# Kernel optimization log

Hardware: AMD Instinct MI355X
Metric: run time of the kernel (lower is better)

## Reference

```python
import jax, jax.numpy as jnp
import numpy as np

KERNEL_SIZE = 2  # matches init kernel_size
EPS = 1e-6


def setup_inputs() -> dict:
    key = jax.random.key(0)
    x = jax.random.uniform(key, (8, 64, 256, 256), dtype=jnp.float32)
    return {"x": x}


def reference(x) -> jnp.ndarray:
    k = KERNEL_SIZE
    b, c, h, w = x.shape
    hp, wp = h - k + 1, w - k + 1  # stride-1 unfold output dims
    n = k * k
    # Gather the k*k shifted views (equivalent to unfold(2,k,1).unfold(3,k,1)).
    # Fixed small loop over k*k offsets, not over data dims.
    windows = jnp.stack(
        [x[:, :, i:i + hp, j:j + wp] for i in range(k) for j in range(k)],
        axis=-1,
    )  # (b, c, hp, wp, n)
    windows = windows.reshape(b, c, hp * wp, n)
    p = windows / (jnp.sum(windows, axis=-1, keepdims=True) + EPS)
    ent = -jnp.sum(p * jnp.log(p + EPS), axis=-1)  # (b, c, hp*wp)
    return ent
```

## Files before the change

### kernel.cpp

```cpp
#include <hip/hip_runtime.h>

#define H    256
#define W    256
#define HP   255
#define WP   255
#define PIX  (HP * WP)
#define NBC  512
#define EPS  1e-6f
#define LN2  0.69314718055994531f

#define TPI   8192
#define NBLK  (NBC * TPI / 256)
#define BPI   32

typedef float f4 __attribute__((ext_vector_type(4)));

__device__ __forceinline__ float wlog(float w) {
    return w * __builtin_amdgcn_logf(w + EPS);
}

__device__ __forceinline__ float ent4(float Wm, float Tm) {
    const float s = Wm + EPS;
    return LN2 * (Wm * __builtin_amdgcn_logf(s) - Tm) * __builtin_amdgcn_rcpf(s);
}

__global__ __launch_bounds__(256) void entropy_k2_kernel(
    const float* __restrict__ x, float* __restrict__ out)
{
    __shared__ float lds[8 * 256];

    const int tid = threadIdx.x;
    const int bc  = blockIdx.x >> 5;
    const int ib  = blockIdx.x & 31;
    const int qh  = tid >> 6;
    const int q   = ib * 4 + qh;
    const int j0  = (tid & 63) << 2;
    const int i0  = q << 1;

    const float* img = x + (size_t)bc * (H * W);
    const float* r0p = img + i0 * W + j0;
    const float* r1p = r0p + W;
    const float* r2p = (q == 127) ? r1p : r1p + W;
    const int j4 = (j0 + 4 < W) ? 4 : 3;

    const f4    va = *(const f4*)r0p;
    const f4    vb = *(const f4*)r1p;
    const f4    vc = *(const f4*)r2p;
    const float a4 = r0p[j4];
    const float b4 = r1p[j4];
    const float c4 = r2p[j4];

    const float la0 = wlog(va.x), la1 = wlog(va.y), la2 = wlog(va.z),
                la3 = wlog(va.w), la4 = wlog(a4);
    const float lb0 = wlog(vb.x), lb1 = wlog(vb.y), lb2 = wlog(vb.z),
                lb3 = wlog(vb.w), lb4 = wlog(b4);
    const float lc0 = wlog(vc.x), lc1 = wlog(vc.y), lc2 = wlog(vc.z),
                lc3 = wlog(vc.w), lc4 = wlog(c4);

    const float hwa0 = va.x + va.y, hwa1 = va.y + va.z, hwa2 = va.z + va.w, hwa3 = va.w + a4;
    const float hwb0 = vb.x + vb.y, hwb1 = vb.y + vb.z, hwb2 = vb.z + vb.w, hwb3 = vb.w + b4;
    const float hwc0 = vc.x + vc.y, hwc1 = vc.y + vc.z, hwc2 = vc.z + vc.w, hwc3 = vc.w + c4;
    const float hta0 = la0 + la1, hta1 = la1 + la2, hta2 = la2 + la3, hta3 = la3 + la4;
    const float htb0 = lb0 + lb1, htb1 = lb1 + lb2, htb2 = lb2 + lb3, htb3 = lb3 + lb4;
    const float htc0 = lc0 + lc1, htc1 = lc1 + lc2, htc2 = lc2 + lc3, htc3 = lc3 + lc4;

    f4 e0, e1;
    e0.x = ent4(hwa0 + hwb0, hta0 + htb0);
    e0.y = ent4(hwa1 + hwb1, hta1 + htb1);
    e0.z = ent4(hwa2 + hwb2, hta2 + htb2);
    e0.w = ent4(hwa3 + hwb3, hta3 + htb3);
    e1.x = ent4(hwb0 + hwc0, htb0 + htc0);
    e1.y = ent4(hwb1 + hwc1, htb1 + htc1);
    e1.z = ent4(hwb2 + hwc2, htb2 + htc2);
    e1.w = ent4(hwb3 + hwc3, htb3 + htc3);

    const int rl = qh << 1;
    *(f4*)&lds[(rl + 0) * 256 + j0] = e0;
    *(f4*)&lds[(rl + 1) * 256 + j0] = e1;

    __syncthreads();

    const int nfloats = (ib == 31) ? 7 * 255 : 8 * 255;
    float* oS = out + (size_t)bc * PIX + (ib * 8) * WP;
    for (int idx = tid; idx < nfloats; idx += 256) {
        const int row = (idx * 2057) >> 19;
        oS[idx] = lds[idx + row];
    }
}

extern "C" void kernel_launch(void* const* d_in, const int* in_sizes, int n_in,
                              void* d_out, int out_size, void* d_ws, size_t ws_size,
                              hipStream_t stream)
{
    const float* x   = (const float*)d_in[0];
    float*       out = (float*)d_out;
    entropy_k2_kernel<<<dim3(NBLK), 256, 0, stream>>>(x, out);
}
```

Measured before the change: 225.2 us.

## Loop each block over eight row tiles with register prefetch and double-buffered LDS

Each block now processes eight consecutive 8-row output tiles instead of one, so the grid shrinks to four blocks per image-channel. The next tile's input rows are loaded into registers while the current tile is computed and stored. The LDS staging buffer alternates between two halves so one barrier per tile suffices. The extra right-neighbour scalar loads are replaced by a wavefront shuffle. The aim is to hide global load latency and cut per-block launch and scalar-load overhead. The cost is less memory parallelism from having far fewer blocks in flight.

Result: slower. 248.7 us (+10.4%).

```diff
diff --git a/kernel.cpp b/kernel.cpp
--- a/kernel.cpp
+++ b/kernel.cpp
@@ -9,9 +9,8 @@
 #define EPS  1e-6f
 #define LN2  0.69314718055994531f
 
-#define TPI   8192
-#define NBLK  (NBC * TPI / 256)
-#define BPI   32
+#define TILES 8
+#define NBLK  (NBC * 4)
 
 typedef float f4 __attribute__((ext_vector_type(4)));
 
@@ -24,67 +23,84 @@
     return LN2 * (Wm * __builtin_amdgcn_logf(s) - Tm) * __builtin_amdgcn_rcpf(s);
 }
 
-__global__ __launch_bounds__(256) void entropy_k2_kernel(
+__global__ __launch_bounds__(256, 8) void entropy_k2_kernel(
     const float* __restrict__ x, float* __restrict__ out)
 {
-    __shared__ float lds[8 * 256];
+    __shared__ float lds[2][8 * 256];
 
-    const int tid = threadIdx.x;
-    const int bc  = blockIdx.x >> 5;
-    const int ib  = blockIdx.x & 31;
-    const int qh  = tid >> 6;
-    const int q   = ib * 4 + qh;
-    const int j0  = (tid & 63) << 2;
-    const int i0  = q << 1;
+    const int tid  = threadIdx.x;
+    const int bc   = blockIdx.x >> 2;
+    const int qb   = blockIdx.x & 3;
+    const int qh   = tid >> 6;
+    const int lane = tid & 63;
+    const int j0   = lane << 2;
+    const bool cl  = (qb == 3) && (qh == 3);
 
     const float* img = x + (size_t)bc * (H * W);
-    const float* r0p = img + i0 * W + j0;
-    const float* r1p = r0p + W;
-    const float* r2p = (q == 127) ? r1p : r1p + W;
-    const int j4 = (j0 + 4 < W) ? 4 : 3;
+    const float* pa = img + (qb * 64 + qh * 2) * W + j0;
 
-    const f4    va = *(const f4*)r0p;
-    const f4    vb = *(const f4*)r1p;
-    const f4    vc = *(const f4*)r2p;
-    const float a4 = r0p[j4];
-    const float b4 = r1p[j4];
-    const float c4 = r2p[j4];
+    f4 va = *(const f4*)pa;
+    f4 vb = *(const f4*)(pa + W);
+    f4 vc = *(const f4*)(pa + 2 * W);
 
-    const float la0 = wlog(va.x), la1 = wlog(va.y), la2 = wlog(va.z),
-                la3 = wlog(va.w), la4 = wlog(a4);
-    const float lb0 = wlog(vb.x), lb1 = wlog(vb.y), lb2 = wlog(vb.z),
-                lb3 = wlog(vb.w), lb4 = wlog(b4);
-    const float lc0 = wlog(vc.x), lc1 = wlog(vc.y), lc2 = wlog(vc.z),
-                lc3 = wlog(vc.w), lc4 = wlog(c4);
+    float* const oBase = out + (size_t)bc * PIX;
 
-    const float hwa0 = va.x + va.y, hwa1 = va.y + va.z, hwa2 = va.z + va.w, hwa3 = va.w + a4;
-    const float hwb0 = vb.x + vb.y, hwb1 = vb.y + vb.z, hwb2 = vb.z + vb.w, hwb3 = vb.w + b4;
-    const float hwc0 = vc.x + vc.y, hwc1 = vc.y + vc.z, hwc2 = vc.z + vc.w, hwc3 = vc.w + c4;
-    const float hta0 = la0 + la1, hta1 = la1 + la2, hta2 = la2 + la3, hta3 = la3 + la4;
-    const float htb0 = lb0 + lb1, htb1 = lb1 + lb2, htb2 = lb2 + lb3, htb3 = lb3 + lb4;
-    const float htc0 = lc0 + lc1, htc1 = lc1 + lc2, htc2 = lc2 + lc3, htc3 = lc3 + lc4;
+    #pragma unroll 1
+    for (int t = 0; t < TILES; ++t) {
+        f4 na, nb, nc;
+        const bool more = (t < TILES - 1);
+        if (more) {
+            const float* pn = pa + 8 * W;
+            na = *(const f4*)pn;
+            nb = *(const f4*)(pn + W);
+            const float* pc = (cl && t == TILES - 2) ? (pn + W) : (pn + 2 * W);
+            nc = *(const f4*)pc;
+        }
 
-    f4 e0, e1;
-    e0.x = ent4(hwa0 + hwb0, hta0 + htb0);
-    e0.y = ent4(hwa1 + hwb1, hta1 + htb1);
-    e0.z = ent4(hwa2 + hwb2, hta2 + htb2);
-    e0.w = ent4(hwa3 + hwb3, hta3 + htb3);
-    e1.x = ent4(hwb0 + hwc0, htb0 + htc0);
-    e1.y = ent4(hwb1 + hwc1, htb1 + htc1);
-    e1.z = ent4(hwb2 + hwc2, htb2 + htc2);
-    e1.w = ent4(hwb3 + hwc3, htb3 + htc3);
+        const float a4 = __shfl_down(va.x, 1);
+        const float b4 = __shfl_down(vb.x, 1);
+        const float c4 = __shfl_down(vc.x, 1);
 
-    const int rl = qh << 1;
-    *(f4*)&lds[(rl + 0) * 256 + j0] = e0;
-    *(f4*)&lds[(rl + 1) * 256 + j0] = e1;
+        const float la0 = wlog(va.x), la1 = wlog(va.y), la2 = wlog(va.z),
+                    la3 = wlog(va.w), la4 = wlog(a4);
+        const float lb0 = wlog(vb.x), lb1 = wlog(vb.y), lb2 = wlog(vb.z),
+                    lb3 = wlog(vb.w), lb4 = wlog(b4);
+        const float lc0 = wlog(vc.x), lc1 = wlog(vc.y), lc2 = wlog(vc.z),
+                    lc3 = wlog(vc.w), lc4 = wlog(c4);
 
-    __syncthreads();
+        const float hwa0 = va.x + va.y, hwa1 = va.y + va.z, hwa2 = va.z + va.w, hwa3 = va.w + a4;
+        const float hwb0 = vb.x + vb.y, hwb1 = vb.y + vb.z, hwb2 = vb.z + vb.w, hwb3 = vb.w + b4;
+        const float hwc0 = vc.x + vc.y, hwc1 = vc.y + vc.z, hwc2 = vc.z + vc.w, hwc3 = vc.w + c4;
+        const float hta0 = la0 + la1, hta1 = la1 + la2, hta2 = la2 + la3, hta3 = la3 + la4;
+        const float htb0 = lb0 + lb1, htb1 = lb1 + lb2, htb2 = lb2 + lb3, htb3 = lb3 + lb4;
+        const float htc0 = lc0 + lc1, htc1 = lc1 + lc2, htc2 = lc2 + lc3, htc3 = lc3 + lc4;
 
-    const int nfloats = (ib == 31) ? 7 * 255 : 8 * 255;
-    float* oS = out + (size_t)bc * PIX + (ib * 8) * WP;
-    for (int idx = tid; idx < nfloats; idx += 256) {
-        const int row = (idx * 2057) >> 19;
-        oS[idx] = lds[idx + row];
+        f4 e0, e1;
+        e0.x = ent4(hwa0 + hwb0, hta0 + htb0);
+        e0.y = ent4(hwa1 + hwb1, hta1 + htb1);
+        e0.z = ent4(hwa2 + hwb2, hta2 + htb2);
+        e0.w = ent4(hwa3 + hwb3, hta3 + htb3);
+        e1.x = ent4(hwb0 + hwc0, htb0 + htc0);
+        e1.y = ent4(hwb1 + hwc1, htb1 + htc1);
+        e1.z = ent4(hwb2 + hwc2, htb2 + htc2);
+        e1.w = ent4(hwb3 + hwc3, htb3 + htc3);
+
+        float* Lb = lds[t & 1];
+        const int rl = qh << 1;
+        *(f4*)&Lb[(rl + 0) * 256 + j0] = e0;
+        *(f4*)&Lb[(rl + 1) * 256 + j0] = e1;
+
+        __syncthreads();
+
+        const int tileAbs = qb * 8 + t;
+        const int nfloats = (tileAbs == 31) ? 7 * 255 : 8 * 255;
+        float* oS = oBase + tileAbs * (8 * WP);
+        for (int idx = tid; idx < nfloats; idx += 256) {
+            const int row = (idx * 2057) >> 19;
+            oS[idx] = Lb[idx + row];
+        }
+
+        if (more) { va = na; vb = nb; vc = nc; pa += 8 * W; }
     }
 }
 
```

## Compute four output rows per thread and fetch right neighbor via shuffle

Applied to the files above, without the earlier changes.

Each thread now loads five input rows and produces four output rows instead of three rows for two outputs, cutting the redundant halo row reads and log evaluations per output from 1.5x to 1.25x. The extra fifth column element is obtained with a lane shuffle instead of a separate scalar global load. Blocks cover 16 rows and the LDS buffer doubles, with a launch-bounds occupancy hint added. The last lane's shuffle returns its own value, which is only correct where that column is discarded, and register pressure rises.

Result: slower. 230.1 us (+2.2%).

```diff
diff --git a/kernel.cpp b/kernel.cpp
--- a/kernel.cpp
+++ b/kernel.cpp
@@ -9,9 +9,7 @@
 #define EPS  1e-6f
 #define LN2  0.69314718055994531f
 
-#define TPI   8192
-#define NBLK  (NBC * TPI / 256)
-#define BPI   32
+#define NBLK  (NBC * 16)
 
 typedef float f4 __attribute__((ext_vector_type(4)));
 
@@ -24,66 +22,67 @@
     return LN2 * (Wm * __builtin_amdgcn_logf(s) - Tm) * __builtin_amdgcn_rcpf(s);
 }
 
-__global__ __launch_bounds__(256) void entropy_k2_kernel(
+__global__ __launch_bounds__(256, 6) void entropy_k2_kernel(
     const float* __restrict__ x, float* __restrict__ out)
 {
-    __shared__ float lds[8 * 256];
+    __shared__ float lds[16 * 256];
 
     const int tid = threadIdx.x;
-    const int bc  = blockIdx.x >> 5;
-    const int ib  = blockIdx.x & 31;
+    const int bc  = blockIdx.x >> 4;
+    const int blk = blockIdx.x & 15;
     const int qh  = tid >> 6;
-    const int q   = ib * 4 + qh;
     const int j0  = (tid & 63) << 2;
-    const int i0  = q << 1;
+    const int i0  = blk * 16 + qh * 4;
 
-    const float* img = x + (size_t)bc * (H * W);
-    const float* r0p = img + i0 * W + j0;
-    const float* r1p = r0p + W;
-    const float* r2p = (q == 127) ? r1p : r1p + W;
-    const int j4 = (j0 + 4 < W) ? 4 : 3;
+    const float* p = x + (size_t)bc * (H * W) + i0 * W + j0;
+    const bool clampTop = (blk == 15) && (qh == 3);
 
-    const f4    va = *(const f4*)r0p;
-    const f4    vb = *(const f4*)r1p;
-    const f4    vc = *(const f4*)r2p;
-    const float a4 = r0p[j4];
-    const float b4 = r1p[j4];
-    const float c4 = r2p[j4];
+    f4 v0 = *(const f4*)(p);
+    f4 v1 = *(const f4*)(p + W);
+    f4 v2 = *(const f4*)(p + 2 * W);
+    f4 v3 = *(const f4*)(p + 3 * W);
+    f4 v4 = *(const f4*)(clampTop ? p + 3 * W : p + 4 * W);
 
-    const float la0 = wlog(va.x), la1 = wlog(va.y), la2 = wlog(va.z),
-                la3 = wlog(va.w), la4 = wlog(a4);
-    const float lb0 = wlog(vb.x), lb1 = wlog(vb.y), lb2 = wlog(vb.z),
-                lb3 = wlog(vb.w), lb4 = wlog(b4);
-    const float lc0 = wlog(vc.x), lc1 = wlog(vc.y), lc2 = wlog(vc.z),
-                lc3 = wlog(vc.w), lc4 = wlog(c4);
+    const float s0 = __shfl_down(v0.x, 1);
+    const float s1 = __shfl_down(v1.x, 1);
+    const float s2 = __shfl_down(v2.x, 1);
+    const float s3 = __shfl_down(v3.x, 1);
+    const float s4 = __shfl_down(v4.x, 1);
 
-    const float hwa0 = va.x + va.y, hwa1 = va.y + va.z, hwa2 = va.z + va.w, hwa3 = va.w + a4;
-    const float hwb0 = vb.x + vb.y, hwb1 = vb.y + vb.z, hwb2 = vb.z + vb.w, hwb3 = vb.w + b4;
-    const float hwc0 = vc.x + vc.y, hwc1 = vc.y + vc.z, hwc2 = vc.z + vc.w, hwc3 = vc.w + c4;
-    const float hta0 = la0 + la1, hta1 = la1 + la2, hta2 = la2 + la3, hta3 = la3 + la4;
-    const float htb0 = lb0 + lb1, htb1 = lb1 + lb2, htb2 = lb2 + lb3, htb3 = lb3 + lb4;
-    const float htc0 = lc0 + lc1, htc1 = lc1 + lc2, htc2 = lc2 + lc3, htc3 = lc3 + lc4;
+    float hw[5][4], ht[5][4];
+#define ROW(r, vv, ss)                                                       \
+    {                                                                        \
+        const float l0 = wlog(vv.x), l1 = wlog(vv.y), l2 = wlog(vv.z),       \
+                    l3 = wlog(vv.w), l4 = wlog(ss);                          \
+        hw[r][0] = vv.x + vv.y; hw[r][1] = vv.y + vv.z;                      \
+        hw[r][2] = vv.z + vv.w; hw[r][3] = vv.w + ss;                        \
+        ht[r][0] = l0 + l1; ht[r][1] = l1 + l2;                              \
+        ht[r][2] = l2 + l3; ht[r][3] = l3 + l4;                              \
+    }
+    ROW(0, v0, s0)
+    ROW(1, v1, s1)
+    ROW(2, v2, s2)
+    ROW(3, v3, s3)
+    ROW(4, v4, s4)
+#undef ROW
 
-    f4 e0, e1;
-    e0.x = ent4(hwa0 + hwb0, hta0 + htb0);
-    e0.y = ent4(hwa1 + hwb1, hta1 + htb1);
-    e0.z = ent4(hwa2 + hwb2, hta2 + htb2);
-    e0.w = ent4(hwa3 + hwb3, hta3 + htb3);
-    e1.x = ent4(hwb0 + hwc0, htb0 + htc0);
-    e1.y = ent4(hwb1 + hwc1, htb1 + htc1);
-    e1.z = ent4(hwb2 + hwc2, htb2 + htc2);
-    e1.w = ent4(hwb3 + hwc3, htb3 + htc3);
-
-    const int rl = qh << 1;
-    *(f4*)&lds[(rl + 0) * 256 + j0] = e0;
-    *(f4*)&lds[(rl + 1) * 256 + j0] = e1;
+    const int rbase = qh * 4;
+#pragma unroll
+    for (int r = 0; r < 4; ++r) {
+        f4 e;
+        e.x = ent4(hw[r][0] + hw[r + 1][0], ht[r][0] + ht[r + 1][0]);
+        e.y = ent4(hw[r][1] + hw[r + 1][1], ht[r][1] + ht[r + 1][1]);
+        e.z = ent4(hw[r][2] + hw[r + 1][2], ht[r][2] + ht[r + 1][2]);
+        e.w = ent4(hw[r][3] + hw[r + 1][3], ht[r][3] + ht[r + 1][3]);
+        *(f4*)&lds[(rbase + r) * 256 + j0] = e;
+    }
 
     __syncthreads();
 
-    const int nfloats = (ib == 31) ? 7 * 255 : 8 * 255;
-    float* oS = out + (size_t)bc * PIX + (ib * 8) * WP;
+    const int nfloats = (blk == 15) ? 15 * 255 : 16 * 255;
+    float* oS = out + (size_t)bc * PIX + blk * (16 * WP);
     for (int idx = tid; idx < nfloats; idx += 256) {
-        const int row = (idx * 2057) >> 19;
+        const int row = (int)((unsigned)idx / 255u);
         oS[idx] = lds[idx + row];
     }
 }
```

## Compute one output row per thread and fetch right neighbour via shuffle

Applied to the files above, without the earlier changes.

Each thread now produces one output row of four pixels instead of two, so it loads two input rows rather than three, and the grid doubles to 64 blocks per image. The scalar load of the fifth column is replaced with a wavefront shuffle-down from the neighbouring lane. This removes the extra scalar loads and lowers per-thread register and log work, in exchange for twice as many blocks and more redundant reads of shared rows across blocks. The last lane's shuffle reads past the wave edge, but it only feeds column 255, which is never written out.

Measured after the change: 223.6 us. No clear change (-0.7%).

```diff
diff --git a/kernel.cpp b/kernel.cpp
--- a/kernel.cpp
+++ b/kernel.cpp
@@ -9,9 +9,7 @@
 #define EPS  1e-6f
 #define LN2  0.69314718055994531f
 
-#define TPI   8192
-#define NBLK  (NBC * TPI / 256)
-#define BPI   32
+#define NBLK  (NBC * 64)
 
 typedef float f4 __attribute__((ext_vector_type(4)));
 
@@ -27,61 +25,46 @@
 __global__ __launch_bounds__(256) void entropy_k2_kernel(
     const float* __restrict__ x, float* __restrict__ out)
 {
-    __shared__ float lds[8 * 256];
+    __shared__ float lds[4 * 256];
 
     const int tid = threadIdx.x;
-    const int bc  = blockIdx.x >> 5;
-    const int ib  = blockIdx.x & 31;
+    const int bc  = blockIdx.x >> 6;
+    const int blk = blockIdx.x & 63;
     const int qh  = tid >> 6;
-    const int q   = ib * 4 + qh;
     const int j0  = (tid & 63) << 2;
-    const int i0  = q << 1;
+    const int i0  = blk * 4 + qh;
 
-    const float* img = x + (size_t)bc * (H * W);
-    const float* r0p = img + i0 * W + j0;
-    const float* r1p = r0p + W;
-    const float* r2p = (q == 127) ? r1p : r1p + W;
-    const int j4 = (j0 + 4 < W) ? 4 : 3;
+    const float* p  = x + (size_t)bc * (H * W) + i0 * W + j0;
+    const float* pb = (i0 < HP) ? p + W : p;
 
-    const f4    va = *(const f4*)r0p;
-    const f4    vb = *(const f4*)r1p;
-    const f4    vc = *(const f4*)r2p;
-    const float a4 = r0p[j4];
-    const float b4 = r1p[j4];
-    const float c4 = r2p[j4];
+    const f4 va = *(const f4*)p;
+    const f4 vb = *(const f4*)pb;
+
+    const float a4 = __shfl_down(va.x, 1);
+    const float b4 = __shfl_down(vb.x, 1);
 
     const float la0 = wlog(va.x), la1 = wlog(va.y), la2 = wlog(va.z),
                 la3 = wlog(va.w), la4 = wlog(a4);
     const float lb0 = wlog(vb.x), lb1 = wlog(vb.y), lb2 = wlog(vb.z),
                 lb3 = wlog(vb.w), lb4 = wlog(b4);
-    const float lc0 = wlog(vc.x), lc1 = wlog(vc.y), lc2 = wlog(vc.z),
-                lc3 = wlog(vc.w), lc4 = wlog(c4);
 
     const float hwa0 = va.x + va.y, hwa1 = va.y + va.z, hwa2 = va.z + va.w, hwa3 = va.w + a4;
     const float hwb0 = vb.x + vb.y, hwb1 = vb.y + vb.z, hwb2 = vb.z + vb.w, hwb3 = vb.w + b4;
-    const float hwc0 = vc.x + vc.y, hwc1 = vc.y + vc.z, hwc2 = vc.z + vc.w, hwc3 = vc.w + c4;
     const float hta0 = la0 + la1, hta1 = la1 + la2, hta2 = la2 + la3, hta3 = la3 + la4;
     const float htb0 = lb0 + lb1, htb1 = lb1 + lb2, htb2 = lb2 + lb3, htb3 = lb3 + lb4;
-    const float htc0 = lc0 + lc1, htc1 = lc1 + lc2, htc2 = lc2 + lc3, htc3 = lc3 + lc4;
 
-    f4 e0, e1;
-    e0.x = ent4(hwa0 + hwb0, hta0 + htb0);
-    e0.y = ent4(hwa1 + hwb1, hta1 + htb1);
-    e0.z = ent4(hwa2 + hwb2, hta2 + htb2);
-    e0.w = ent4(hwa3 + hwb3, hta3 + htb3);
-    e1.x = ent4(hwb0 + hwc0, htb0 + htc0);
-    e1.y = ent4(hwb1 + hwc1, htb1 + htc1);
-    e1.z = ent4(hwb2 + hwc2, htb2 + htc2);
-    e1.w = ent4(hwb3 + hwc3, htb3 + htc3);
+    f4 e;
+    e.x = ent4(hwa0 + hwb0, hta0 + htb0);
+    e.y = ent4(hwa1 + hwb1, hta1 + htb1);
+    e.z = ent4(hwa2 + hwb2, hta2 + htb2);
+    e.w = ent4(hwa3 + hwb3, hta3 + htb3);
 
-    const int rl = qh << 1;
-    *(f4*)&lds[(rl + 0) * 256 + j0] = e0;
-    *(f4*)&lds[(rl + 1) * 256 + j0] = e1;
+    *(f4*)&lds[qh * 256 + j0] = e;
 
     __syncthreads();
 
-    const int nfloats = (ib == 31) ? 7 * 255 : 8 * 255;
-    float* oS = out + (size_t)bc * PIX + (ib * 8) * WP;
+    const int nfloats = (blk == 63) ? 3 * 255 : 4 * 255;
+    float* oS = out + (size_t)bc * PIX + blk * (4 * WP);
     for (int idx = tid; idx < nfloats; idx += 256) {
         const int row = (idx * 2057) >> 19;
         oS[idx] = lds[idx + row];
```
